# Performance work log

Hardware: AMD Instinct MI355X
Metric: run time of the kernel (lower is better)

The kernel has to match this reference:

```python
import jax, jax.numpy as jnp
import numpy as np

TOPK = 10
NUM_CLASSES = 80
ALPHA = 1.0
BETA = 6.0
EPS = 1e-8


def setup_inputs() -> dict:
    key = jax.random.key(0)
    ks = jax.random.split(key, 6)
    B, A, NB, C = 32, 8400, 32, 80
    pred_scores = jax.random.uniform(ks[0], (B, A, C), dtype=jnp.float32)
    # anchor grid for 640x640 image, strides 8/16/32 -> 6400+1600+400 = 8400 points
    pts = []
    for s in (8, 16, 32):
        n = 640 // s
        xs = (jnp.arange(n, dtype=jnp.float32) + 0.5) * s
        gy, gx = jnp.meshgrid(xs, xs, indexing='ij')
        pts.append(jnp.stack([gx.ravel(), gy.ravel()], axis=-1))
    anchor_points = jnp.concatenate(pts, axis=0)  # (8400, 2)
    # predicted boxes: anchor point +- random extents (xyxy)
    off = jax.random.uniform(ks[1], (B, A, 4), minval=4.0, maxval=64.0, dtype=jnp.float32)
    pred_boxes = jnp.concatenate([anchor_points[None] - off[..., :2],
                                  anchor_points[None] + off[..., 2:]], axis=-1)
    gt_cxcy = jax.random.uniform(ks[2], (B, NB, 2), minval=64.0, maxval=576.0, dtype=jnp.float32)
    gt_wh = jax.random.uniform(ks[3], (B, NB, 2), minval=16.0, maxval=256.0, dtype=jnp.float32)
    gt_boxes = jnp.concatenate([gt_cxcy - gt_wh / 2, gt_cxcy + gt_wh / 2], axis=-1)
    gt_labels = jax.random.randint(ks[4], (B, NB, 1), 0, C)
    gt_mask = jax.random.uniform(ks[5], (B, NB, 1)) < 0.8  # padded-GT validity mask
    return {"pred_scores": pred_scores, "pred_boxes": pred_boxes,
            "anchor_points": anchor_points, "gt_labels": gt_labels,
            "gt_boxes": gt_boxes, "gt_mask": gt_mask}


def reference(pred_scores, pred_boxes, anchor_points, gt_labels, gt_boxes, gt_mask):
    B, A, C = pred_scores.shape
    NB = gt_boxes.shape[1]
    dt = pred_scores.dtype
    gt_valid = gt_mask[..., 0]  # (B, NB) bool

    # --- step 3 mask: anchor centers inside GT boxes ---
    lt = gt_boxes[:, :, None, :2]  # (B, NB, 1, 2)
    rb = gt_boxes[:, :, None, 2:]
    ap = anchor_points[None, None]  # (1, 1, A, 2)
    d = jnp.minimum((ap - lt).min(-1), (rb - ap).min(-1))  # (B, NB, A)
    mask_in = d > 1e-8
    valid = mask_in & gt_valid[:, :, None]
    vf = valid.astype(dt)

    # --- classification score of each anchor for each GT's class ---
    cls = gt_labels[..., 0].astype(jnp.int32)  # (B, NB)
    bcs = jnp.take_along_axis(pred_scores, cls[:, None, :], axis=2)  # (B, A, NB)
    bcs = jnp.swapaxes(bcs, 1, 2) * vf  # (B, NB, A)

    # --- pairwise IoU (xyxy) between GT and predicted boxes ---
    b1 = gt_boxes[:, :, None, :]   # (B, NB, 1, 4)
    b2 = pred_boxes[:, None, :, :]  # (B, 1, A, 4)
    iw = jnp.clip(jnp.minimum(b1[..., 2], b2[..., 2]) - jnp.maximum(b1[..., 0], b2[..., 0]), 0)
    ih = jnp.clip(jnp.minimum(b1[..., 3], b2[..., 3]) - jnp.maximum(b1[..., 1], b2[..., 1]), 0)
    inter = iw * ih
    a1 = (b1[..., 2] - b1[..., 0]) * (b1[..., 3] - b1[..., 1])
    a2 = (b2[..., 2] - b2[..., 0]) * (b2[..., 3] - b2[..., 1])
    ious = jnp.maximum(inter / (a1 + a2 - inter + 1e-10), 0.0) * vf  # (B, NB, A)

    align = jnp.power(bcs, ALPHA) * jnp.power(ious, BETA)  # (B, NB, A)

    # --- step 2: top-k candidates per GT (scatter-add counts, drop dupes) ---
    _, topk_idx = jax.lax.top_k(align, TOPK)  # (B, NB, K)
    topk_idx = jnp.where(gt_valid[:, :, None], topk_idx, 0)
    bi = jnp.arange(B)[:, None, None]
    gi = jnp.arange(NB)[None, :, None]
    counts = jnp.zeros((B, NB, A), jnp.int32).at[bi, gi, topk_idx].add(1)
    topk_mask = jnp.where(counts > 1, 0, counts).astype(dt)
    mask = topk_mask * vf  # (B, NB, A)

    # --- step 4: anchors matched to multiple GTs keep the highest-IoU GT ---
    fg = mask.sum(axis=1)  # (B, A)
    best_gt = jnp.argmax(ious, axis=1)  # (B, A)
    onehot_best = (best_gt[:, None, :] == jnp.arange(NB)[None, :, None]).astype(dt)
    mask = jnp.where(fg[:, None, :] > 1, onehot_best, mask)
    fg = mask.sum(axis=1)
    tgt_idx = jnp.argmax(mask, axis=1)  # (B, A)

    # --- gather targets ---
    target_labels = jnp.clip(jnp.take_along_axis(cls, tgt_idx, axis=1), 0, NUM_CLASSES)  # (B, A)
    target_boxes = jnp.take_along_axis(gt_boxes, tgt_idx[..., None], axis=1)  # (B, A, 4)
    target_scores = jax.nn.one_hot(target_labels, NUM_CLASSES, dtype=dt)
    target_scores = target_scores * (fg[..., None] > 0)

    # --- normalize scores by aligned metric ---
    align = align * mask
    pos_align = align.max(axis=-1, keepdims=True)           # (B, NB, 1)
    pos_iou = (ious * mask).max(axis=-1, keepdims=True)     # (B, NB, 1)
    norm = (align * pos_iou / (pos_align + EPS)).max(axis=-2)[..., None]  # (B, A, 1)
    target_scores = target_scores * norm

    return target_labels, target_boxes, target_scores, fg > 0
```

## Files before the change

### kernel.cpp

```cpp
#include <hip/hip_runtime.h>
#include <cstdint>
#include <cstddef>

#define BB 32
#define AA 8400
#define NBB 32
#define CC 80
#define TOPKN 10

typedef float nfloat4 __attribute__((ext_vector_type(4)));

__global__ __launch_bounds__(256) void gt_topk_kernel(
    const float* __restrict__ pred_scores, const float* __restrict__ pred_boxes,
    const int* __restrict__ gt_labels, const float* __restrict__ gt_boxes,
    const int* __restrict__ gt_mask,
    int* __restrict__ tk, int* __restrict__ posA, int* __restrict__ posI,
    float* __restrict__ out) {
  const int j = blockIdx.x, b = blockIdx.y, t = threadIdx.x;
  const int g = b * NBB + j;

  if (blockIdx.z == 1) {
    const int NA = BB * AA;
    const int labels4 = NA / 4;
    const int boxes4_end = labels4 + NA;
    const int total4 = labels4 + NA + NA * 20 + NA / 4;
    nfloat4* o4 = reinterpret_cast<nfloat4*>(out);
    for (int idx = (g << 8) + t; idx < total4; idx += 1024 * 256) {
      nfloat4 v;
      if (idx < labels4) {
        const int fb = (idx * 4) / AA;
        int lab = gt_labels[fb * NBB];
        lab = min(max(lab, 0), 80);
        const float lf = (float)lab;
        v = (nfloat4){lf, lf, lf, lf};
      } else if (idx < boxes4_end) {
        const int aidx = idx - labels4;
        const int fb = aidx / AA;
        v = *reinterpret_cast<const nfloat4*>(gt_boxes + (size_t)fb * NBB * 4);
      } else {
        v = (nfloat4){0.f, 0.f, 0.f, 0.f};
      }
      __builtin_nontemporal_store(v, &o4[idx]);
    }
    return;
  }

  if (t == 0) { posA[g] = 0; posI[g] = 0; }

  const float gx0 = gt_boxes[g * 4 + 0], gy0 = gt_boxes[g * 4 + 1];
  const float gx1 = gt_boxes[g * 4 + 2], gy1 = gt_boxes[g * 4 + 3];
  const int cls = gt_labels[g];
  const bool valid = (gt_mask[g] != 0);
  const float ga1 = (gx1 - gx0) * (gy1 - gy0);

  unsigned long long tkkey[TOPKN];
#pragma unroll
  for (int k = 0; k < TOPKN; k++) tkkey[k] = 0ull;

  if (valid) {
    const int strides[3] = {8, 16, 32};
    const int grids[3] = {80, 40, 20};
    const int offs[3] = {0, 6400, 8000};
    for (int lvl = 0; lvl < 3; lvl++) {
      const float s = (float)strides[lvl];
      const int n = grids[lvl], off = offs[lvl];
      int lx = max(0, (int)floorf(gx0 / s - 0.5f) - 1);
      int hx = min(n - 1, (int)ceilf(gx1 / s - 0.5f) + 1);
      int ly = max(0, (int)floorf(gy0 / s - 0.5f) - 1);
      int hy = min(n - 1, (int)ceilf(gy1 / s - 0.5f) + 1);
      if (hx < lx || hy < ly) continue;
      const int w = hx - lx + 1;
      const int m = w * (hy - ly + 1);
      for (int i = t; i < m; i += 256) {
        const int ix = lx + i % w;
        const int iy = ly + i / w;
        const float apx = ((float)ix + 0.5f) * s;
        const float apy = ((float)iy + 0.5f) * s;
        const float d = fminf(fminf(apx - gx0, apy - gy0),
                              fminf(gx1 - apx, gy1 - apy));
        if (!(d > 1e-8f)) continue;
        const int a = off + iy * n + ix;
        const float* pb = pred_boxes + ((size_t)b * AA + a) * 4;
        const float p0 = pb[0], p1 = pb[1], p2 = pb[2], p3 = pb[3];
        const float iw = fmaxf(fminf(gx1, p2) - fmaxf(gx0, p0), 0.0f);
        const float ih = fmaxf(fminf(gy1, p3) - fmaxf(gy0, p1), 0.0f);
        const float inter = iw * ih;
        const float a2 = (p2 - p0) * (p3 - p1);
        const float iou = fmaxf(inter / (ga1 + a2 - inter + 1e-10f), 0.0f);
        const float sc = pred_scores[((size_t)b * AA + a) * CC + cls];
        const float i2 = iou * iou;
        const float align_v = sc * i2 * i2 * i2;
        const unsigned long long key =
            ((unsigned long long)__float_as_uint(align_v) << 32) |
            (unsigned int)(AA - a);
        if (key > tkkey[TOPKN - 1]) {
          tkkey[TOPKN - 1] = key;
#pragma unroll
          for (int k = TOPKN - 1; k > 0; k--) {
            if (tkkey[k] > tkkey[k - 1]) {
              unsigned long long tmp = tkkey[k];
              tkkey[k] = tkkey[k - 1];
              tkkey[k - 1] = tmp;
            }
          }
        }
      }
    }
  }

  __shared__ unsigned long long s_key[256][TOPKN + 1];
#pragma unroll
  for (int k = 0; k < TOPKN; k++) s_key[t][k] = tkkey[k];
  __syncthreads();

  for (int stride = 128; stride >= 1; stride >>= 1) {
    if (t < stride) {
      unsigned long long mk[TOPKN];
      int p = 0, q = 0;
#pragma unroll
      for (int k = 0; k < TOPKN; k++) {
        const unsigned long long k1 = s_key[t][p], k2 = s_key[t + stride][q];
        if (k1 >= k2) { mk[k] = k1; p++; } else { mk[k] = k2; q++; }
      }
#pragma unroll
      for (int k = 0; k < TOPKN; k++) s_key[t][k] = mk[k];
    }
    __syncthreads();
  }

  if (t < TOPKN) {
    const unsigned long long key = s_key[0][t];
    tk[g * TOPKN + t] = (key != 0ull) ? (AA - (int)(key & 0xffffffffu)) : -1;
  }
}

__global__ __launch_bounds__(64) void assign_sparse_kernel(
    const float* __restrict__ pred_scores, const float* __restrict__ pred_boxes,
    const float* __restrict__ anchor_points, const int* __restrict__ gt_labels,
    const float* __restrict__ gt_boxes, const int* __restrict__ gt_mask,
    const int* __restrict__ tk,
    int* __restrict__ resj, float* __restrict__ resAl,
    int* __restrict__ posA, int* __restrict__ posI) {
  const int j = blockIdx.x, b = blockIdx.y, t = threadIdx.x;

  __shared__ float sbox[NBB][4];
  __shared__ int scls[NBB];
  __shared__ int svalid[NBB];
  __shared__ int sa[NBB * TOPKN];

  if (t < NBB) {
    const int g = b * NBB + t;
    sbox[t][0] = gt_boxes[g * 4 + 0];
    sbox[t][1] = gt_boxes[g * 4 + 1];
    sbox[t][2] = gt_boxes[g * 4 + 2];
    sbox[t][3] = gt_boxes[g * 4 + 3];
    scls[t] = gt_labels[g];
    svalid[t] = (gt_mask[g] != 0) ? 1 : 0;
  }
  for (int e = t; e < NBB * TOPKN; e += 64) sa[e] = tk[b * NBB * TOPKN + e];
  __syncthreads();

  if (t >= TOPKN) return;
  const int a = sa[j * TOPKN + t];
  if (a < 0) return;

  int cnt = 0;
  for (int q = 0; q < NBB * TOPKN; q++) cnt += (sa[q] == a) ? 1 : 0;

  const float apx = anchor_points[a * 2 + 0];
  const float apy = anchor_points[a * 2 + 1];
  const float* pb = pred_boxes + ((size_t)b * AA + a) * 4;
  const float p0 = pb[0], p1 = pb[1], p2 = pb[2], p3 = pb[3];
  const float a2 = (p2 - p0) * (p3 - p1);

  int jj;
  float iou_f;
  if (cnt == 1) {
    jj = j;
    const float gx0 = sbox[j][0], gy0 = sbox[j][1];
    const float gx1 = sbox[j][2], gy1 = sbox[j][3];
    const float iw = fmaxf(fminf(gx1, p2) - fmaxf(gx0, p0), 0.0f);
    const float ih = fmaxf(fminf(gy1, p3) - fmaxf(gy0, p1), 0.0f);
    const float inter = iw * ih;
    const float a1 = (gx1 - gx0) * (gy1 - gy0);
    iou_f = fmaxf(inter / (a1 + a2 - inter + 1e-10f), 0.0f);
  } else {
    float best_iou = -1.0f;
    int best_j = 0;
    for (int jq = 0; jq < NBB; jq++) {
      const float gx0 = sbox[jq][0], gy0 = sbox[jq][1];
      const float gx1 = sbox[jq][2], gy1 = sbox[jq][3];
      const float d = fminf(fminf(apx - gx0, apy - gy0),
                            fminf(gx1 - apx, gy1 - apy));
      float iou = 0.0f;
      if (svalid[jq] && d > 1e-8f) {
        const float iw = fmaxf(fminf(gx1, p2) - fmaxf(gx0, p0), 0.0f);
        const float ih = fmaxf(fminf(gy1, p3) - fmaxf(gy0, p1), 0.0f);
        const float inter = iw * ih;
        const float a1 = (gx1 - gx0) * (gy1 - gy0);
        iou = fmaxf(inter / (a1 + a2 - inter + 1e-10f), 0.0f);
      }
      if (iou > best_iou) { best_iou = iou; best_j = jq; }
    }
    jj = best_j;
    iou_f = best_iou;
  }

  const float sc = pred_scores[((size_t)b * AA + a) * CC + scls[jj]];
  const float i2 = iou_f * iou_f;
  const float align_v = sc * i2 * i2 * i2;
  const int e = (b * NBB + j) * TOPKN + t;
  resj[e] = jj;
  resAl[e] = align_v;
  atomicMax(&posA[b * NBB + jj], __float_as_int(align_v));
  atomicMax(&posI[b * NBB + jj], __float_as_int(iou_f));
}

__global__ __launch_bounds__(256) void scatter_out_kernel(
    const int* __restrict__ gt_labels, const float* __restrict__ gt_boxes,
    const int* __restrict__ tk, const int* __restrict__ resj,
    const float* __restrict__ resAl, const int* __restrict__ posA,
    const int* __restrict__ posI, float* __restrict__ out) {
  const int e = blockIdx.x * 256 + threadIdx.x;
  if (e >= BB * NBB * TOPKN) return;
  const int a = tk[e];
  if (a < 0) return;
  const int b = e / (NBB * TOPKN);
  const int jj = resj[e];
  const float align_v = resAl[e];
  const float pa = __int_as_float(posA[b * NBB + jj]);
  const float pi = __int_as_float(posI[b * NBB + jj]);
  const float norm = align_v * pi / (pa + 1e-8f);
  int label = gt_labels[b * NBB + jj];
  label = min(max(label, 0), 80);
  const size_t aidx = (size_t)b * AA + a;

  out[aidx] = (float)label;
  *reinterpret_cast<float4*>(out + (size_t)BB * AA + aidx * 4) =
      *reinterpret_cast<const float4*>(gt_boxes + ((size_t)b * NBB + jj) * 4);
  if (label < CC)
    out[(size_t)BB * AA * 5 + aidx * CC + label] = norm;
  out[(size_t)BB * AA * 85 + aidx] = 1.0f;
}

extern "C" void kernel_launch(void* const* d_in, const int* in_sizes, int n_in,
                              void* d_out, int out_size, void* d_ws, size_t ws_size,
                              hipStream_t stream) {
  const float* pred_scores = (const float*)d_in[0];
  const float* pred_boxes = (const float*)d_in[1];
  const float* anchor_points = (const float*)d_in[2];
  const int* gt_labels = (const int*)d_in[3];
  const float* gt_boxes = (const float*)d_in[4];
  const int* gt_mask = (const int*)d_in[5];
  float* out = (float*)d_out;
  char* ws = (char*)d_ws;

  const size_t off_tk = 0;
  const size_t off_posA = off_tk + (size_t)BB * NBB * TOPKN * 4;
  const size_t off_posI = off_posA + 4096;
  const size_t off_resj = off_posI + 4096;
  const size_t off_resAl = off_resj + (size_t)BB * NBB * TOPKN * 4;

  int* tk = (int*)(ws + off_tk);
  int* posA = (int*)(ws + off_posA);
  int* posI = (int*)(ws + off_posI);
  int* resj = (int*)(ws + off_resj);
  float* resAl = (float*)(ws + off_resAl);

  dim3 g1(NBB, BB, 2);
  gt_topk_kernel<<<g1, 256, 0, stream>>>(pred_scores, pred_boxes, gt_labels,
                                         gt_boxes, gt_mask, tk, posA, posI,
                                         out);

  dim3 g2(NBB, BB);
  assign_sparse_kernel<<<g2, 64, 0, stream>>>(
      pred_scores, pred_boxes, anchor_points, gt_labels, gt_boxes, gt_mask,
      tk, resj, resAl, posA, posI);

  const int ncand = BB * NBB * TOPKN;
  scatter_out_kernel<<<(ncand + 255) / 256, 256, 0, stream>>>(
      gt_labels, gt_boxes, tk, resj, resAl, posA, posI, out);
}
```

Before: 47.09 us.

## Shrink top-k blocks to one wavefront and merge with shuffle butterfly

The per-GT top-k kernel now runs one 64-thread wavefront per block instead of 256 threads. The shared-memory tree merge of per-thread top-10 lists, which needed a barrier at every level, is replaced by a register-only XOR butterfly. Each step pairs two sorted lists into a bitonic max and re-sorts it with odd-even transposition. This removes shared memory use and block barriers, but each thread now scans four times as many candidate anchors. The output zero/fill half of the grid also has four times fewer threads issuing stores, which may lower memory-level parallelism on the large output write.

Measured after the change: 48.43 us. 1.03x slower.

```diff
diff --git a/kernel.cpp b/kernel.cpp
--- a/kernel.cpp
+++ b/kernel.cpp
@@ -10,7 +10,14 @@
 
 typedef float nfloat4 __attribute__((ext_vector_type(4)));
 
-__global__ __launch_bounds__(256) void gt_topk_kernel(
+__device__ __forceinline__ unsigned long long shfl_u64(unsigned long long v,
+                                                       int src) {
+  const int lo = __shfl((int)(v & 0xffffffffull), src, 64);
+  const int hi = __shfl((int)(v >> 32), src, 64);
+  return ((unsigned long long)(unsigned int)hi << 32) | (unsigned int)lo;
+}
+
+__global__ __launch_bounds__(64) void gt_topk_kernel(
     const float* __restrict__ pred_scores, const float* __restrict__ pred_boxes,
     const int* __restrict__ gt_labels, const float* __restrict__ gt_boxes,
     const int* __restrict__ gt_mask,
@@ -25,7 +32,7 @@
     const int boxes4_end = labels4 + NA;
     const int total4 = labels4 + NA + NA * 20 + NA / 4;
     nfloat4* o4 = reinterpret_cast<nfloat4*>(out);
-    for (int idx = (g << 8) + t; idx < total4; idx += 1024 * 256) {
+    for (int idx = (g << 6) + t; idx < total4; idx += 1024 * 64) {
       nfloat4 v;
       if (idx < labels4) {
         const int fb = (idx * 4) / AA;
@@ -71,7 +78,7 @@
       if (hx < lx || hy < ly) continue;
       const int w = hx - lx + 1;
       const int m = w * (hy - ly + 1);
-      for (int i = t; i < m; i += 256) {
+      for (int i = t; i < m; i += 64) {
         const int ix = lx + i % w;
         const int iy = ly + i / w;
         const float apx = ((float)ix + 0.5f) * s;
@@ -108,28 +115,35 @@
     }
   }
 
-  __shared__ unsigned long long s_key[256][TOPKN + 1];
-#pragma unroll
-  for (int k = 0; k < TOPKN; k++) s_key[t][k] = tkkey[k];
-  __syncthreads();
-
-  for (int stride = 128; stride >= 1; stride >>= 1) {
-    if (t < stride) {
-      unsigned long long mk[TOPKN];
-      int p = 0, q = 0;
-#pragma unroll
-      for (int k = 0; k < TOPKN; k++) {
-        const unsigned long long k1 = s_key[t][p], k2 = s_key[t + stride][q];
-        if (k1 >= k2) { mk[k] = k1; p++; } else { mk[k] = k2; q++; }
-      }
-#pragma unroll
-      for (int k = 0; k < TOPKN; k++) s_key[t][k] = mk[k];
-    }
-    __syncthreads();
+#pragma unroll
+  for (int s = 1; s < 64; s <<= 1) {
+    const int partner = t ^ s;
+    unsigned long long other[TOPKN];
+#pragma unroll
+    for (int k = 0; k < TOPKN; k++) other[k] = shfl_u64(tkkey[k], partner);
+    unsigned long long L[TOPKN];
+#pragma unroll
+    for (int k = 0; k < TOPKN; k++) {
+      const unsigned long long o = other[TOPKN - 1 - k];
+      L[k] = (tkkey[k] > o) ? tkkey[k] : o;
+    }
+#pragma unroll
+    for (int r = 0; r < TOPKN; r++) {
+#pragma unroll
+      for (int k = (r & 1); k + 1 < TOPKN; k += 2) {
+        if (L[k] < L[k + 1]) {
+          const unsigned long long tmp = L[k];
+          L[k] = L[k + 1];
+          L[k + 1] = tmp;
+        }
+      }
+    }
+#pragma unroll
+    for (int k = 0; k < TOPKN; k++) tkkey[k] = L[k];
   }
 
   if (t < TOPKN) {
-    const unsigned long long key = s_key[0][t];
+    const unsigned long long key = tkkey[t];
     tk[g * TOPKN + t] = (key != 0ull) ? (AA - (int)(key & 0xffffffffu)) : -1;
   }
 }
@@ -268,9 +282,9 @@
   float* resAl = (float*)(ws + off_resAl);
 
   dim3 g1(NBB, BB, 2);
-  gt_topk_kernel<<<g1, 256, 0, stream>>>(pred_scores, pred_boxes, gt_labels,
-                                         gt_boxes, gt_mask, tk, posA, posI,
-                                         out);
+  gt_topk_kernel<<<g1, 64, 0, stream>>>(pred_scores, pred_boxes, gt_labels,
+                                        gt_boxes, gt_mask, tk, posA, posI,
+                                        out);
 
   dim3 g2(NBB, BB);
   assign_sparse_kernel<<<g2, 64, 0, stream>>>(
```
